# Optimization experiments

Measured on AMD Instinct MI355X. Metric: run time of the kernel, lower is better.

## Reference

```python
import jax, jax.numpy as jnp
import numpy as np

N = 8192       # node_num
F_IN = 256     # src_feature
F_OUT = 128    # out_feature
NEG_SLOPE = 0.2  # standard GAT leakyrelu slope
MASK_VAL = -1e12


def setup_inputs() -> dict:
    key = jax.random.key(0)
    k1, k2, k3, k4, k5, k6 = jax.random.split(key, 6)
    x = jax.random.normal(k1, (N, F_IN), dtype=jnp.float32)
    adj = jax.random.randint(k2, (N, N), 0, 2, dtype=jnp.int32)  # 0/1 adjacency mask
    # xavier-uniform-like scales
    W = jax.random.normal(k3, (F_IN, F_OUT), dtype=jnp.float32) * np.float32(1.0 / np.sqrt(F_IN))
    a1 = jax.random.normal(k4, (F_OUT,), dtype=jnp.float32) * np.float32(0.1)  # att[:F_OUT]
    a2 = jax.random.normal(k5, (F_OUT,), dtype=jnp.float32) * np.float32(0.1)  # att[F_OUT:]
    bias = jax.random.normal(k6, (F_OUT,), dtype=jnp.float32) * np.float32(0.1)
    return {"x": x, "adj": adj, "W": W, "a1": a1, "a2": a2, "bias": bias}


def reference(x, adj, W, a1, a2, bias):
    # h = x @ W1  (src_h == dst_h for int src_dst_feature)
    h = x @ W  # [N, F_OUT]
    # e[i,j] = leakyrelu(att^T [h_i || h_j]) decomposed as (h@a1)_i + (h@a2)_j
    s_src = h @ a1  # [N]
    s_dst = h @ a2  # [N]
    e = jax.nn.leaky_relu(s_src[:, None] + s_dst[None, :], NEG_SLOPE)  # [N, N]
    masked = jnp.where(adj > 0, e, jnp.float32(MASK_VAL))
    attention = jax.nn.softmax(masked, axis=1)  # [N, N]
    # dropout in eval mode = identity; aggregate neighbor features
    out = attention @ h + bias  # [N, F_OUT]
    return out
```

## Files before the change

kernel.cpp:

```cpp
#include <hip/hip_runtime.h>
#include <cstdint>
#include <cstddef>

#define NN 8192
#define FIN 256
#define FOUT 128
#define SLOPE 0.2f
#define SHIFT 8.0f

typedef float f32x4 __attribute__((ext_vector_type(4)));
typedef __bf16 bf16x8 __attribute__((ext_vector_type(8)));
typedef int i32x4 __attribute__((ext_vector_type(4)));
typedef unsigned int u32x4 __attribute__((ext_vector_type(4)));

__device__ __forceinline__ unsigned short f2bf(float f) {
  return __builtin_bit_cast(unsigned short, (__bf16)f);
}
__device__ __forceinline__ float bf2f(unsigned short u) {
  return (float)__builtin_bit_cast(__bf16, u);
}

__device__ __forceinline__ void async_cp16(void* lds, const void* g) {
  __builtin_amdgcn_global_load_lds(
      (const __attribute__((address_space(1))) void*)g,
      (__attribute__((address_space(3))) void*)lds, 16, 0, 0);
}

__global__ __launch_bounds__(256, 4) void k_hw(const float* __restrict__ x,
                                               const float* __restrict__ W,
                                               const float* __restrict__ a1,
                                               const float* __restrict__ a2,
                                               unsigned short* __restrict__ ht,
                                               float* __restrict__ Etab,
                                               unsigned short* __restrict__ Fbf) {
  __shared__ float xs[8][256];
  __shared__ unsigned short tile[128][8];
  const int tid = threadIdx.x;
  const int rowbase = blockIdx.x * 8;

  #pragma unroll
  for (int it = 0; it < 2; ++it) {
    int fi = it * 1024 + tid * 4;
    int r = fi >> 8, k = fi & 255;
    *(f32x4*)&xs[r][k] = *(const f32x4*)(x + (size_t)(rowbase + r) * FIN + k);
  }
  __syncthreads();

  const int r = tid >> 5;
  const int cg = tid & 31;
  f32x4 acc = {0.f, 0.f, 0.f, 0.f};

  #pragma unroll 8
  for (int k = 0; k < FIN; ++k) {
    f32x4 wv = *(const f32x4*)(W + k * FOUT + cg * 4);
    float xv = xs[r][k];
    acc[0] += xv * wv[0];
    acc[1] += xv * wv[1];
    acc[2] += xv * wv[2];
    acc[3] += xv * wv[3];
  }

  #pragma unroll
  for (int c = 0; c < 4; ++c) tile[cg * 4 + c][r] = f2bf(acc[c]);

  f32x4 av1 = *(const f32x4*)(a1 + cg * 4);
  f32x4 av2 = *(const f32x4*)(a2 + cg * 4);
  float s1 = acc[0] * av1[0] + acc[1] * av1[1] + acc[2] * av1[2] + acc[3] * av1[3];
  float s2 = acc[0] * av2[0] + acc[1] * av2[1] + acc[2] * av2[2] + acc[3] * av2[3];
  #pragma unroll
  for (int off = 16; off > 0; off >>= 1) {
    s1 += __shfl_xor(s1, off, 64);
    s2 += __shfl_xor(s2, off, 64);
  }
  if (cg == 0) {
    const int row = rowbase + r;
    float c0 = s1 + SHIFT;
    float c = fmaxf(c0, SLOPE * c0);
    f32x4 ev;
    ev[0] = __expf(s1 - c);
    ev[1] = __expf(SLOPE * s1 - c);
    ev[2] = __expf(-s1);
    ev[3] = 0.f;
    *(f32x4*)(Etab + (size_t)row * 4) = ev;
    Fbf[(size_t)row * 2]     = f2bf(__expf(s2));
    Fbf[(size_t)row * 2 + 1] = f2bf(__expf(SLOPE * s2));
  }
  __syncthreads();

  if (tid < 128) {
    u32x4 v = *(const u32x4*)&tile[tid][0];
    *(u32x4*)(ht + (size_t)tid * NN + rowbase) = v;
  }
}

__global__ __launch_bounds__(256, 2) void k_gat(const int* __restrict__ adj,
                                                const unsigned short* __restrict__ ht,
                                                const float* __restrict__ Etab,
                                                const unsigned short* __restrict__ Fbf,
                                                const float* __restrict__ bias,
                                                float* __restrict__ out) {
  __shared__ int sA[2][16 * 64];
  __shared__ unsigned short sH[2][128 * 64];
  __shared__ unsigned short sF[2][128];

  const int tid = threadIdx.x;
  const int wave = tid >> 6;
  const int lane = tid & 63;
  const int quad = lane >> 4;
  const int m = lane & 15;
  const int rowbase = blockIdx.x * 16;
  const int row = rowbase + m;

  bf16x8 pm, pinv, pones;
  #pragma unroll
  for (int jj = 0; jj < 8; ++jj) {
    pm[jj] = (__bf16)(float)m;
    pinv[jj] = (__bf16)0.03125f;
    pones[jj] = (__bf16)1.0f;
  }
  f32x4 z = {0.f, 0.f, 0.f, 0.f};
  f32x4 rp = __builtin_amdgcn_mfma_f32_16x16x32_bf16(pm, pinv, z, 0, 0, 0);
  f32x4 cp = __builtin_amdgcn_mfma_f32_16x16x32_bf16(pinv, pm, z, 0, 0, 0);
  int rowmap[4], colmap[4];
  #pragma unroll
  for (int r = 0; r < 4; ++r) {
    rowmap[r] = ((int)(rp[r] + 0.5f)) & 15;
    colmap[r] = ((int)(cp[r] + 0.5f)) & 15;
  }

  f32x4 ev = *(const f32x4*)(Etab + (size_t)row * 4);
  const float E = ev[0], E2 = ev[1], Einv = ev[2];

  const int t0 = wave * 2, t1 = wave * 2 + 1;

  f32x4 acc0 = z, acc1 = z, den = z;

  auto stage = [&](int c, int b) {
    #pragma unroll
    for (int il = 0; il < 4; ++il) {
      const int i = wave * 4 + il;
      const int f = i * 8 + (lane >> 3);
      const int g = (lane & 7) ^ (lane >> 3);
      async_cp16(&sH[b][i * 512],
                 ht + (size_t)f * NN + c * 64 + g * 8);
    }
    if (wave == 0) {
      #pragma unroll
      for (int il = 0; il < 4; ++il) {
        const int r = il * 4 + (lane >> 4);
        const int g = (lane & 15) ^ r;
        async_cp16(&sA[b][il * 256],
                   adj + (size_t)(rowbase + r) * NN + c * 64 + g * 4);
      }
    } else if (wave == 1 && lane < 16) {
      async_cp16(&sF[b][0], Fbf + (size_t)c * 128 + lane * 8);
    }
  };

  stage(0, 0);
  __syncthreads();

  for (int c = 0; c < 128; ++c) {
    const int cs = c & 1, ns = cs ^ 1;
    if (c + 1 < 128) stage(c + 1, ns);

    #pragma unroll
    for (int k32 = 0; k32 < 2; ++k32) {
      const int g0 = k32 * 8 + quad * 2;
      i32x4 A0 = *(const i32x4*)&sA[cs][m * 64 + ((g0) ^ m) * 4];
      i32x4 A1 = *(const i32x4*)&sA[cs][m * 64 + ((g0 + 1) ^ m) * 4];
      u32x4 Fq0 = *(const u32x4*)&sF[cs][g0 * 8];
      u32x4 Fq1 = *(const u32x4*)&sF[cs][(g0 + 1) * 8];

      bf16x8 af;
      #pragma unroll
      for (int jj = 0; jj < 8; ++jj) {
        const u32x4& Fq = (jj < 4) ? Fq0 : Fq1;
        const unsigned pk = Fq[jj & 3];
        float F  = bf2f((unsigned short)(pk & 0xffffu));
        float F2 = bf2f((unsigned short)(pk >> 16));
        int av = (jj < 4) ? A0[jj] : A1[jj - 4];
        bool pos = (F >= Einv);
        float w = (pos ? E : E2) * (pos ? F : F2);
        af[jj] = (av != 0) ? (__bf16)w : (__bf16)0.0f;
      }

      const int gp = k32 * 4 + quad;
      const int s0 = gp ^ (m & 7);
      bf16x8 b0 = __builtin_bit_cast(bf16x8,
          *(const u32x4*)&sH[cs][(t0 * 16 + m) * 64 + s0 * 8]);
      bf16x8 b1 = __builtin_bit_cast(bf16x8,
          *(const u32x4*)&sH[cs][(t1 * 16 + m) * 64 + s0 * 8]);

      acc0 = __builtin_amdgcn_mfma_f32_16x16x32_bf16(af, b0, acc0, 0, 0, 0);
      acc1 = __builtin_amdgcn_mfma_f32_16x16x32_bf16(af, b1, acc1, 0, 0, 0);
      den  = __builtin_amdgcn_mfma_f32_16x16x32_bf16(af, pones, den, 0, 0, 0);
    }
    __syncthreads();
  }

  #pragma unroll
  for (int r = 0; r < 4; ++r) {
    const float inv = 1.0f / den[r];
    const int orow = rowbase + rowmap[r];
    const int c0 = t0 * 16 + colmap[r];
    const int c1 = t1 * 16 + colmap[r];
    out[(size_t)orow * FOUT + c0] = acc0[r] * inv + bias[c0];
    out[(size_t)orow * FOUT + c1] = acc1[r] * inv + bias[c1];
  }
}

extern "C" void kernel_launch(void* const* d_in, const int* in_sizes, int n_in,
                              void* d_out, int out_size, void* d_ws, size_t ws_size,
                              hipStream_t stream) {
  const float* x    = (const float*)d_in[0];
  const int*   adj  = (const int*)d_in[1];
  const float* W    = (const float*)d_in[2];
  const float* a1   = (const float*)d_in[3];
  const float* a2   = (const float*)d_in[4];
  const float* bias = (const float*)d_in[5];
  float* out = (float*)d_out;

  char* ws = (char*)d_ws;
  unsigned short* ht = (unsigned short*)ws;
  float* Etab = (float*)(ws + (size_t)2 * 1024 * 1024);
  unsigned short* Fbf =
      (unsigned short*)(ws + (size_t)2 * 1024 * 1024 + 128 * 1024);

  k_hw<<<NN / 8, 256, 0, stream>>>(x, W, a1, a2, ht, Etab, Fbf);
  k_gat<<<NN / 16, 256, 0, stream>>>(adj, ht, Etab, Fbf, bias, out);
}
```

Measured before the change: 484.6 us.

## Split F tables, use max-based leakyrelu weight, rebalance loads and move barrier

```diff
diff --git a/kernel.cpp b/kernel.cpp
--- a/kernel.cpp
+++ b/kernel.cpp
@@ -15,9 +15,6 @@
 
 __device__ __forceinline__ unsigned short f2bf(float f) {
   return __builtin_bit_cast(unsigned short, (__bf16)f);
-}
-__device__ __forceinline__ float bf2f(unsigned short u) {
-  return (float)__builtin_bit_cast(__bf16, u);
 }
 
 __device__ __forceinline__ void async_cp16(void* lds, const void* g) {
@@ -32,7 +29,8 @@
                                                const float* __restrict__ a2,
                                                unsigned short* __restrict__ ht,
                                                float* __restrict__ Etab,
-                                               unsigned short* __restrict__ Fbf) {
+                                               unsigned short* __restrict__ FbfF,
+                                               unsigned short* __restrict__ FbfF2) {
   __shared__ float xs[8][256];
   __shared__ unsigned short tile[128][8];
   const int tid = threadIdx.x;
@@ -76,14 +74,10 @@
     const int row = rowbase + r;
     float c0 = s1 + SHIFT;
     float c = fmaxf(c0, SLOPE * c0);
-    f32x4 ev;
-    ev[0] = __expf(s1 - c);
-    ev[1] = __expf(SLOPE * s1 - c);
-    ev[2] = __expf(-s1);
-    ev[3] = 0.f;
-    *(f32x4*)(Etab + (size_t)row * 4) = ev;
-    Fbf[(size_t)row * 2]     = f2bf(__expf(s2));
-    Fbf[(size_t)row * 2 + 1] = f2bf(__expf(SLOPE * s2));
+    Etab[(size_t)row * 2]     = __expf(s1 - c);
+    Etab[(size_t)row * 2 + 1] = __expf(SLOPE * s1 - c);
+    FbfF[row]  = f2bf(__expf(s2));
+    FbfF2[row] = f2bf(__expf(SLOPE * s2));
   }
   __syncthreads();
 
@@ -96,7 +90,8 @@
 __global__ __launch_bounds__(256, 2) void k_gat(const int* __restrict__ adj,
                                                 const unsigned short* __restrict__ ht,
                                                 const float* __restrict__ Etab,
-                                                const unsigned short* __restrict__ Fbf,
+                                                const unsigned short* __restrict__ FbfF,
+                                                const unsigned short* __restrict__ FbfF2,
                                                 const float* __restrict__ bias,
                                                 float* __restrict__ out) {
   __shared__ int sA[2][16 * 64];
@@ -128,65 +123,90 @@
     colmap[r] = ((int)(cp[r] + 0.5f)) & 15;
   }
 
-  f32x4 ev = *(const f32x4*)(Etab + (size_t)row * 4);
-  const float E = ev[0], E2 = ev[1], Einv = ev[2];
+  const float E  = Etab[(size_t)row * 2];
+  const float E2 = Etab[(size_t)row * 2 + 1];
 
   const int t0 = wave * 2, t1 = wave * 2 + 1;
 
   f32x4 acc0 = z, acc1 = z, den = z;
 
-  auto stage = [&](int c, int b) {
+  const unsigned short* srcH[4];
+  #pragma unroll
+  for (int il = 0; il < 4; ++il) {
+    const int i = wave * 4 + il;
+    const int f = i * 8 + (lane >> 3);
+    const int g = (lane & 7) ^ (lane >> 3);
+    srcH[il] = ht + (size_t)f * NN + g * 8;
+  }
+  const int* srcA[2] = {nullptr, nullptr};
+  int slotA[2] = {0, 0};
+  if (wave >= 2) {
+    #pragma unroll
+    for (int q = 0; q < 2; ++q) {
+      const int il = (wave - 2) * 2 + q;
+      const int r = il * 4 + (lane >> 4);
+      const int g = (lane & 15) ^ r;
+      slotA[q] = il;
+      srcA[q] = adj + (size_t)(rowbase + r) * NN + g * 4;
+    }
+  }
+  const unsigned short* srcF = nullptr;
+  if (wave == 1) {
+    srcF = (lane < 8) ? (FbfF + lane * 8) : (FbfF2 + (lane - 8) * 8);
+  }
+
+  auto stage = [&](int b) {
     #pragma unroll
     for (int il = 0; il < 4; ++il) {
-      const int i = wave * 4 + il;
-      const int f = i * 8 + (lane >> 3);
-      const int g = (lane & 7) ^ (lane >> 3);
-      async_cp16(&sH[b][i * 512],
-                 ht + (size_t)f * NN + c * 64 + g * 8);
-    }
-    if (wave == 0) {
+      async_cp16(&sH[b][(wave * 4 + il) * 512], srcH[il]);
+      srcH[il] += 64;
+    }
+    if (wave >= 2) {
       #pragma unroll
-      for (int il = 0; il < 4; ++il) {
-        const int r = il * 4 + (lane >> 4);
-        const int g = (lane & 15) ^ r;
-        async_cp16(&sA[b][il * 256],
-                   adj + (size_t)(rowbase + r) * NN + c * 64 + g * 4);
+      for (int q = 0; q < 2; ++q) {
+        async_cp16(&sA[b][slotA[q] * 256], srcA[q]);
+        srcA[q] += 64;
       }
     } else if (wave == 1 && lane < 16) {
-      async_cp16(&sF[b][0], Fbf + (size_t)c * 128 + lane * 8);
+      async_cp16(&sF[b][0], srcF);
+      srcF += 64;
     }
   };
 
-  stage(0, 0);
-  __syncthreads();
+  stage(0);
 
   for (int c = 0; c < 128; ++c) {
     const int cs = c & 1, ns = cs ^ 1;
-    if (c + 1 < 128) stage(c + 1, ns);
+
+    __syncthreads();
+    if (c + 1 < 128) stage(ns);
 
     #pragma unroll
     for (int k32 = 0; k32 < 2; ++k32) {
       const int g0 = k32 * 8 + quad * 2;
       i32x4 A0 = *(const i32x4*)&sA[cs][m * 64 + ((g0) ^ m) * 4];
       i32x4 A1 = *(const i32x4*)&sA[cs][m * 64 + ((g0 + 1) ^ m) * 4];
-      u32x4 Fq0 = *(const u32x4*)&sF[cs][g0 * 8];
-      u32x4 Fq1 = *(const u32x4*)&sF[cs][(g0 + 1) * 8];
+      const int jl = k32 * 32 + quad * 8;
+      u32x4 Fq = *(const u32x4*)&sF[cs][jl];
+      u32x4 Gq = *(const u32x4*)&sF[cs][64 + jl];
 
       bf16x8 af;
       #pragma unroll
-      for (int jj = 0; jj < 8; ++jj) {
-        const u32x4& Fq = (jj < 4) ? Fq0 : Fq1;
-        const unsigned pk = Fq[jj & 3];
-        float F  = bf2f((unsigned short)(pk & 0xffffu));
-        float F2 = bf2f((unsigned short)(pk >> 16));
-        int av = (jj < 4) ? A0[jj] : A1[jj - 4];
-        bool pos = (F >= Einv);
-        float w = (pos ? E : E2) * (pos ? F : F2);
-        af[jj] = (av != 0) ? (__bf16)w : (__bf16)0.0f;
+      for (int p = 0; p < 4; ++p) {
+        const unsigned fp = Fq[p], gp = Gq[p];
+        const float Flo = __builtin_bit_cast(float, fp << 16);
+        const float Fhi = __builtin_bit_cast(float, fp & 0xffff0000u);
+        const float Glo = __builtin_bit_cast(float, gp << 16);
+        const float Ghi = __builtin_bit_cast(float, gp & 0xffff0000u);
+        const float wlo = fmaxf(E * Flo, E2 * Glo);
+        const float whi = fmaxf(E * Fhi, E2 * Ghi);
+        const int avlo = (p < 2) ? A0[p * 2] : A1[p * 2 - 4];
+        const int avhi = (p < 2) ? A0[p * 2 + 1] : A1[p * 2 - 3];
+        af[p * 2]     = avlo ? (__bf16)wlo : (__bf16)0.0f;
+        af[p * 2 + 1] = avhi ? (__bf16)whi : (__bf16)0.0f;
       }
 
-      const int gp = k32 * 4 + quad;
-      const int s0 = gp ^ (m & 7);
+      const int s0 = (k32 * 4 + quad) ^ (m & 7);
       bf16x8 b0 = __builtin_bit_cast(bf16x8,
           *(const u32x4*)&sH[cs][(t0 * 16 + m) * 64 + s0 * 8]);
       bf16x8 b1 = __builtin_bit_cast(bf16x8,
@@ -196,7 +216,6 @@
       acc1 = __builtin_amdgcn_mfma_f32_16x16x32_bf16(af, b1, acc1, 0, 0, 0);
       den  = __builtin_amdgcn_mfma_f32_16x16x32_bf16(af, pones, den, 0, 0, 0);
     }
-    __syncthreads();
   }
 
   #pragma unroll
@@ -224,9 +243,10 @@
   char* ws = (char*)d_ws;
   unsigned short* ht = (unsigned short*)ws;
   float* Etab = (float*)(ws + (size_t)2 * 1024 * 1024);
-  unsigned short* Fbf =
-      (unsigned short*)(ws + (size_t)2 * 1024 * 1024 + 128 * 1024);
-
-  k_hw<<<NN / 8, 256, 0, stream>>>(x, W, a1, a2, ht, Etab, Fbf);
-  k_gat<<<NN / 16, 256, 0, stream>>>(adj, ht, Etab, Fbf, bias, out);
-}
+  unsigned short* FbfF =
+      (unsigned short*)(ws + (size_t)2 * 1024 * 1024 + 64 * 1024);
+  unsigned short* FbfF2 = FbfF + NN;
+
+  k_hw<<<NN / 8, 256, 0, stream>>>(x, W, a1, a2, ht, Etab, FbfF, FbfF2);
+  k_gat<<<NN / 16, 256, 0, stream>>>(adj, ht, Etab, FbfF, FbfF2, bias, out);
+}
```

Result: no change. 478.1 us (-1.3%).
